# Performance work log

Hardware: AMD Instinct MI355X
Metric: run time of the kernel (lower is better)

Reference implementation:

```python
import jax, jax.numpy as jnp
import numpy as np

N_LAYERS = 2
D = 128


def _prelu(z, a):
    return jnp.where(z >= 0, z, a * z)


def _seg_sum(vals, idx, num):
    return jax.ops.segment_sum(vals, idx, num_segments=num)


def _conv_layer(x, ni, ei, Wn2e, bn2e, We2n, be2n, alpha, Dn_inv, De_inv, num_nodes, num_edges):
    # node -> edge: mean over member nodes (row norm), then linear + bias + PReLU
    e = _seg_sum((x @ Wn2e)[ni] * De_inv[ei][:, None], ei, num_edges) + bn2e
    e = _prelu(e, alpha)
    # edge -> node: mean over incident hyperedges
    n = _seg_sum((e @ We2n)[ei] * Dn_inv[ni][:, None], ni, num_nodes) + be2n
    return n, e


def _encoder(x, ni, ei, Wn2e, bn2e, We2n, be2n, alpha, Dn_inv, De_inv, num_nodes, num_edges):
    e = None
    for i in range(N_LAYERS):
        x, e = _conv_layer(x, ni, ei, Wn2e[i], bn2e[i], We2n[i], be2n[i], alpha, Dn_inv, De_inv, num_nodes, num_edges)
        x = _prelu(x, alpha)
    return x, e


def _decoder(x, e, ni, ei, We, Wx, b, alpha, Dn_inv, num_nodes):
    for i in range(N_LAYERS):
        m = _seg_sum((e @ We[i])[ei] * Dn_inv[ni][:, None], ni, num_nodes)
        x = _prelu(x @ Wx[i] + m + b[i], alpha)
    return x


def _forward(x, xx,
             e1_Wn2e, e1_bn2e, e1_We2n, e1_be2n,
             e2_Wn2e, e2_bn2e, e2_We2n, e2_be2n,
             d1_We, d1_Wx, d1_b, d2_We, d2_Wx, d2_b,
             alpha, node_idx, edge_idx, num_nodes, num_edges):
    # self loops: each node gets its own private hyperedge (id num_edges + node_id)
    ni = jnp.concatenate([node_idx, jnp.arange(num_nodes, dtype=node_idx.dtype)])
    ei = jnp.concatenate([edge_idx, jnp.arange(num_edges, num_edges + num_nodes, dtype=edge_idx.dtype)])
    ne_tot = num_edges + num_nodes
    ones = jnp.ones(ni.shape[0], x.dtype)
    Dn = _seg_sum(ones, ni, num_nodes)
    De = _seg_sum(ones, ei, ne_tot)
    Dn_inv = jnp.where(Dn > 0, 1.0 / Dn, 0.0)
    De_inv = jnp.where(De > 0, 1.0 / De, 0.0)

    n1, e1 = _encoder(x, ni, ei, e1_Wn2e, e1_bn2e, e1_We2n, e1_be2n, alpha, Dn_inv, De_inv, num_nodes, ne_tot)
    n2, e2 = _encoder(xx, ni, ei, e2_Wn2e, e2_bn2e, e2_We2n, e2_be2n, alpha, Dn_inv, De_inv, num_nodes, ne_tot)

    x11 = _decoder(n1, e1, ni, ei, d1_We, d1_Wx, d1_b, alpha, Dn_inv, num_nodes)
    x21 = _decoder(n2, e2, ni, ei, d2_We, d2_Wx, d2_b, alpha, Dn_inv, num_nodes)
    x12 = _decoder(n2, e2, ni, ei, d1_We, d1_Wx, d1_b, alpha, Dn_inv, num_nodes)
    x22 = _decoder(n1, e1, ni, ei, d2_We, d2_Wx, d2_b, alpha, Dn_inv, num_nodes)

    nn1 = jnp.concatenate([n1, n2], axis=1)
    return (nn1, n1, e1[:num_edges], n2, e2[:num_edges], x11, x21, x12, x22)


def setup_inputs() -> dict:
    key = jax.random.key(0)
    ks = jax.random.split(key, 24)
    N, E, NNZ = 50000, 20000, 800000
    s = 1.0 / np.sqrt(D)
    inp = {
        'x': jax.random.normal(ks[0], (N, D), jnp.float32),
        'xx': jax.random.normal(ks[1], (N, D), jnp.float32),
        'node_idx': jax.random.randint(ks[2], (NNZ,), 0, N, jnp.int32),
        'edge_idx': jax.random.randint(ks[3], (NNZ,), 0, E, jnp.int32),
        'num_nodes': N,
        'num_edges': E,
        'alpha': jnp.float32(0.25),
    }
    i = 4
    for enc in ('e1', 'e2'):
        inp[enc + '_Wn2e'] = jax.random.normal(ks[i], (N_LAYERS, D, D), jnp.float32) * s; i += 1
        inp[enc + '_bn2e'] = jnp.zeros((N_LAYERS, D), jnp.float32)
        inp[enc + '_We2n'] = jax.random.normal(ks[i], (N_LAYERS, D, D), jnp.float32) * s; i += 1
        inp[enc + '_be2n'] = jnp.zeros((N_LAYERS, D), jnp.float32)
    for dec in ('d1', 'd2'):
        inp[dec + '_We'] = jax.random.normal(ks[i], (N_LAYERS, D, D), jnp.float32) * s; i += 1
        inp[dec + '_Wx'] = jax.random.normal(ks[i], (N_LAYERS, D, D), jnp.float32) * s; i += 1
        inp[dec + '_b'] = jnp.zeros((N_LAYERS, D), jnp.float32)
    return inp


def reference(x, xx,
              e1_Wn2e, e1_bn2e, e1_We2n, e1_be2n,
              e2_Wn2e, e2_bn2e, e2_We2n, e2_be2n,
              d1_We, d1_Wx, d1_b, d2_We, d2_Wx, d2_b,
              alpha, node_idx, edge_idx, num_nodes, num_edges):
    return _forward(x, xx,
                    e1_Wn2e, e1_bn2e, e1_We2n, e1_be2n,
                    e2_Wn2e, e2_bn2e, e2_We2n, e2_be2n,
                    d1_We, d1_Wx, d1_b, d2_We, d2_Wx, d2_b,
                    alpha, node_idx, edge_idx, num_nodes, num_edges)
```

## Files before the change

kernel.cpp:

```cpp
#include <hip/hip_runtime.h>

#define DD 128

typedef __attribute__((ext_vector_type(8))) short bh8;
typedef __attribute__((ext_vector_type(8))) unsigned short us8;
typedef __attribute__((ext_vector_type(4))) float f4;
typedef unsigned int u32;
typedef unsigned short u16;

__device__ __forceinline__ u16 tob(float f) {
  u32 u = __builtin_bit_cast(u32, f);
  u += 0x7FFFu + ((u >> 16) & 1u);
  return (u16)(u >> 16);
}
__device__ __forceinline__ float fb(u16 h) { return __builtin_bit_cast(float, (u32)h << 16); }


__global__ __launch_bounds__(256) void init_counts_k(int* cn, int* ce, int N, int E) {
  int g = blockIdx.x * blockDim.x + threadIdx.x;
  if (g < E) ce[g] = 0;
  if (g < N) cn[g] = 0;
}


__global__ __launch_bounds__(256) void scan_partials_k(const int* __restrict__ cn, const int* __restrict__ ce,
                                                       int* part, int NCHN, int N, int NCHE, int E) {
  __shared__ int red[256];
  int b = blockIdx.x, tid = threadIdx.x;
  const int* cnt = (b < NCHN) ? cn : ce;
  int n = (b < NCHN) ? N : E;
  int base = ((b < NCHN) ? b : (b - NCHN)) << 10;
  int i0 = base + tid * 4;
  int s = 0;
  #pragma unroll
  for (int j = 0; j < 4; ++j) { int i = i0 + j; if (i < n) s += cnt[i]; }
  red[tid] = s; __syncthreads();
  for (int off = 128; off > 0; off >>= 1) {
    if (tid < off) red[tid] += red[tid + off];
    __syncthreads();
  }
  if (tid == 0) part[b] = red[0];
}

__device__ __forceinline__ int blk_excl_scan(int s, int tid, int* sums) {
  sums[tid] = s; __syncthreads();
  for (int off = 1; off < 256; off <<= 1) {
    int t = (tid >= off) ? sums[tid - off] : 0;
    __syncthreads();
    sums[tid] += t;
    __syncthreads();
  }
  int ex = sums[tid] - s;
  __syncthreads();
  return ex;
}

__global__ __launch_bounds__(256) void scan_apply_k(const int* __restrict__ cn, const int* __restrict__ ce,
                                                    const int* __restrict__ part,
                                                    int* offs_n, int* offs_e,
                                                    int NCHN, int N, int NCHE, int E) {
  __shared__ int sums[256];
  __shared__ int base_s;
  int b = blockIdx.x, tid = threadIdx.x;
  const bool isN = b < NCHN;
  const int* cnt = isN ? cn : ce;
  int* offs = isN ? offs_n : offs_e;
  int n = isN ? N : E;
  int nch = isN ? NCHN : NCHE;
  int c = isN ? b : b - NCHN;
  const int* pbase = isN ? part : part + NCHN;
  {
    int v = (tid < nch) ? pbase[tid] : 0;
    int ex = blk_excl_scan(v, tid, sums);
    if (tid == c) base_s = ex;
  }
  __syncthreads();
  int base = (c << 10);
  int i0 = base + tid * 4;
  int v[4]; int s = 0;
  #pragma unroll
  for (int j = 0; j < 4; ++j) { int i = i0 + j; int t = (i < n) ? cnt[i] : 0; v[j] = t; s += t; }
  int ex = blk_excl_scan(s, tid, sums);
  int run = base_s + ex;
  #pragma unroll
  for (int j = 0; j < 4; ++j) { int i = i0 + j; if (i < n) offs[i] = run; run += v[j]; }
  if (tid == 255 && base + 1024 >= n) offs[n] = run;
}

__global__ __launch_bounds__(256) void fill_deg_k(const int* __restrict__ offs_n, const int* __restrict__ offs_e,
                                                  float* Dn_inv, float* De_inv,
                                                  int* cur_be, int* cur_bn,
                                                  int N, int E, int NBE, int NBN) {
  int g = blockIdx.x * blockDim.x + threadIdx.x;
  if (g < E) {
    int b = offs_e[g], e = offs_e[g + 1];
    De_inv[g] = (e > b) ? 1.0f / (float)(e - b) : 0.0f;
  }
  if (g < N) {
    int b = offs_n[g], e = offs_n[g + 1];
    Dn_inv[g] = 1.0f / (float)(e - b + 1);
  }
  if (g < NBE) {
    int r1 = (g + 1) * 32; if (r1 > E) r1 = E;
    int o0 = offs_e[g * 32], o1 = offs_e[r1];
    int C = o1 - o0, base = 8 * o0;
    #pragma unroll
    for (int k = 0; k < 8; ++k) cur_be[g * 8 + k] = base + k * C;
  }
  if (g < NBN) {
    int r1 = (g + 1) * 32; if (r1 > N) r1 = N;
    int o0 = offs_n[g * 32], o1 = offs_n[r1];
    int C = o1 - o0, base = 8 * o0;
    #pragma unroll
    for (int k = 0; k < 8; ++k) cur_bn[g * 8 + k] = base + k * C;
  }
}

__global__ __launch_bounds__(256) void partition2_k(const int* __restrict__ ni, const int* __restrict__ ei,
                                                    int* cur_be, int* cur_bn,
                                                    u32* __restrict__ SE, u32* __restrict__ SN, int nnz) {
  int xcd;
  asm volatile("s_getreg_b32 %0, hwreg(HW_REG_XCC_ID)" : "=s"(xcd));
  xcd &= 7;
  int stride = gridDim.x * blockDim.x;
  for (int j = blockIdx.x * blockDim.x + threadIdx.x; j < nnz; j += stride) {
    int n = ni[j], e = ei[j];
    int pe = atomicAdd(&cur_be[(e >> 5) * 8 + xcd], 1);
    SE[pe] = ((u32)(e & 31) << 17) | (u32)n;
    int pn = atomicAdd(&cur_bn[(n >> 5) * 8 + xcd], 1);
    SN[pn] = ((u32)(n & 31) << 17) | (u32)e;
  }
}

__device__ __forceinline__ void scatter_body(const u32* __restrict__ S, const int* __restrict__ offs,
                                             const int* __restrict__ cur_b,
                                             int* __restrict__ list, int nRows, int b, int tid, int* cur) {
  const int i0 = b << 5;
  if (tid < 32) {
    int row = i0 + tid;
    cur[tid] = (row < nRows) ? offs[row] : 0;
  }
  __syncthreads();
  int r1 = i0 + 32; if (r1 > nRows) r1 = nRows;
  const int o0 = offs[i0];
  const int C = offs[r1] - o0;
  #pragma unroll 1
  for (int k = 0; k < 8; ++k) {
    int sbeg = 8 * o0 + k * C;
    int send = cur_b[b * 8 + k];
    for (int i = sbeg + tid; i < send; i += 256) {
      u32 v = S[i];
      int pos = atomicAdd(&cur[v >> 17], 1);
      list[pos] = (int)(v & 0x1FFFFu);
    }
  }
}

__global__ __launch_bounds__(256) void scatter_both_k(const u32* SE, const int* offs_e, const int* cur_be,
                                                      int* listE, int E, int NBE,
                                                      const u32* SN, const int* offs_n, const int* cur_bn,
                                                      int* listN, int N) {
  __shared__ int cur[32];
  int b = blockIdx.x, tid = threadIdx.x;
  if (b < NBE) scatter_body(SE, offs_e, cur_be, listE, E, b, tid, cur);
  else         scatter_body(SN, offs_n, cur_bn, listN, N, b - NBE, tid, cur);
}


__device__ __forceinline__ void acc8(float a[8], us8 v) {
  #pragma unroll
  for (int j = 0; j < 8; ++j) a[j] += fb(v[j]);
}

template<int SPLIT>
__global__ __launch_bounds__(256) void gather_edge_k(const u16* __restrict__ srcb,
                                                     const int* __restrict__ offs, const int* __restrict__ list,
                                                     const float* __restrict__ De_inv,
                                                     const float* __restrict__ b1, const float* __restrict__ b2,
                                                     const float* __restrict__ alphap,
                                                     u16* __restrict__ e_fullb,
                                                     float* __restrict__ d2a, float* __restrict__ d2b, int E) {
  const int wave = threadIdx.x >> 6, lane = threadIdx.x & 63;
  const int row = blockIdx.x * 4 + wave;
  if (row >= E) return;
  const int half = lane >> 5, cl = lane & 31;
  const int c8 = cl * 8;
  const int beg = offs[row], end = offs[row + 1];
  float a0[8] = {0,0,0,0,0,0,0,0}, a1[8] = {0,0,0,0,0,0,0,0};
  int i = beg + half;
  for (; i + 2 < end; i += 4) {
    us8 v0 = *(const us8*)&srcb[(size_t)list[i] * 256 + c8];
    us8 v1 = *(const us8*)&srcb[(size_t)list[i + 2] * 256 + c8];
    acc8(a0, v0); acc8(a1, v1);
  }
  if (i < end) acc8(a0, *(const us8*)&srcb[(size_t)list[i] * 256 + c8]);
  float s[8];
  #pragma unroll
  for (int j = 0; j < 8; ++j) s[j] = a0[j] + a1[j];
  #pragma unroll
  for (int j = 0; j < 8; ++j) s[j] += __shfl_xor(s[j], 32);
  if (half == 0) {
    float sc = De_inv[row];
    const float* bp = (c8 < 128) ? (b1 + c8) : (b2 + c8 - 128);
    float4 bt0 = *(const float4*)bp;
    float4 bt1 = *(const float4*)(bp + 4);
    float bb[8] = {bt0.x, bt0.y, bt0.z, bt0.w, bt1.x, bt1.y, bt1.z, bt1.w};
    float al = *alphap;
    us8 ob;
    float ov[8];
    #pragma unroll
    for (int j = 0; j < 8; ++j) {
      float v = sc * s[j] + bb[j];
      v = (v >= 0.f) ? v : al * v;
      ov[j] = v; ob[j] = tob(v);
    }
    *(us8*)&e_fullb[(size_t)row * 256 + c8] = ob;
    if constexpr (SPLIT == 1) {
      float* dp = (c8 < 128) ? &d2a[(size_t)row * DD + c8] : &d2b[(size_t)row * DD + c8 - 128];
      float4 w0 = {ov[0], ov[1], ov[2], ov[3]};
      float4 w1 = {ov[4], ov[5], ov[6], ov[7]};
      *(float4*)dp = w0;
      *(float4*)(dp + 4) = w1;
    }
  }
}

__global__ __launch_bounds__(256) void gather_node_k(const u16* __restrict__ e_fullb,
                                                     const u16* __restrict__ tb,
                                                     const int* __restrict__ offs, const int* __restrict__ list,
                                                     const float* __restrict__ Dn_inv,
                                                     const float* __restrict__ b1, const float* __restrict__ b2,
                                                     const float* __restrict__ alphap,
                                                     u16* __restrict__ dstb, int N) {
  const int wave = threadIdx.x >> 6, lane = threadIdx.x & 63;
  const int row = blockIdx.x * 4 + wave;
  if (row >= N) return;
  const int half = lane >> 5, cl = lane & 31;
  const int c8 = cl * 8;
  const int beg = offs[row], end = offs[row + 1];
  float a0[8] = {0,0,0,0,0,0,0,0}, a1[8] = {0,0,0,0,0,0,0,0};
  int i = beg + half;
  for (; i + 2 < end; i += 4) {
    us8 v0 = *(const us8*)&e_fullb[(size_t)list[i] * 256 + c8];
    us8 v1 = *(const us8*)&e_fullb[(size_t)list[i + 2] * 256 + c8];
    acc8(a0, v0); acc8(a1, v1);
  }
  if (i < end) acc8(a0, *(const us8*)&e_fullb[(size_t)list[i] * 256 + c8]);
  float s[8];
  #pragma unroll
  for (int j = 0; j < 8; ++j) s[j] = a0[j] + a1[j];
  #pragma unroll
  for (int j = 0; j < 8; ++j) s[j] += __shfl_xor(s[j], 32);
  if (half == 0) {
    us8 tv = *(const us8*)&tb[(size_t)row * 256 + c8];
    const float* bp = (c8 < 128) ? (b1 + c8) : (b2 + c8 - 128);
    float4 bt0 = *(const float4*)bp;
    float4 bt1 = *(const float4*)(bp + 4);
    float bb[8] = {bt0.x, bt0.y, bt0.z, bt0.w, bt1.x, bt1.y, bt1.z, bt1.w};
    float al = *alphap;
    float sc = Dn_inv[row];
    us8 ob;
    #pragma unroll
    for (int j = 0; j < 8; ++j) {
      float sv = fb(tv[j]) + bb[j];
      sv = (sv >= 0.f) ? sv : al * sv;
      ob[j] = tob(sc * (sv + s[j]));
    }
    *(us8*)&dstb[(size_t)row * 256 + c8] = ob;
  }
}


struct WPtrs { const float* p[16]; };

__global__ __launch_bounds__(256) void prep_w_k(WPtrs wp, char* dst) {
  int m = blockIdx.x >> 3, s = blockIdx.x & 7;
  const float* W = wp.p[m];
  int t = threadIdx.x;
  int n = t & 127;
  int k0 = s * 16 + (t >> 7) * 8;
  us8 vhi, vlo;
  #pragma unroll
  for (int j = 0; j < 8; ++j) {
    float x = W[(size_t)(k0 + j) * DD + n];
    u32 ux = __builtin_bit_cast(u32, x);
    float hf = __builtin_bit_cast(float, ux & 0xFFFF0000u);
    float l = x - hf;
    vhi[j] = (u16)(ux >> 16);
    vlo[j] = (u16)(__builtin_bit_cast(u32, l) >> 16);
  }
  char* base = dst + (size_t)m * 65536;
  int byte = n * 256 + k0 * 2;
  byte ^= (n & 7) << 4;
  *(us8*)(base + byte) = vhi;
  *(us8*)(base + 32768 + byte) = vlo;
}


__device__ __forceinline__ void stage_w(const char* gsrc, char* lds, int tid) {
  int wave = tid >> 6, lane = tid & 63;
  #pragma unroll
  for (int i = 0; i < 16; ++i) {
    int off = (wave * 16 + i) * 1024;
    __builtin_amdgcn_global_load_lds(
        (const __attribute__((address_space(1))) u32*)(gsrc + off + lane * 16),
        (__attribute__((address_space(3))) u32*)(lds + off), 16, 0, 0);
  }
}

__device__ __forceinline__ void stage_w32(const char* gsrc, char* lds, int tid) {
  int wave = tid >> 6, lane = tid & 63;
  #pragma unroll
  for (int i = 0; i < 8; ++i) {
    int off = (wave * 8 + i) * 1024;
    __builtin_amdgcn_global_load_lds(
        (const __attribute__((address_space(1))) u32*)(gsrc + off + lane * 16),
        (__attribute__((address_space(3))) u32*)(lds + off), 16, 0, 0);
  }
}

__device__ __forceinline__ void split8(const float vs[8], bh8& hi, bh8& lo) {
  #pragma unroll
  for (int j = 0; j < 8; ++j) {
    u32 u = __builtin_bit_cast(u32, vs[j]);
    float hf = __builtin_bit_cast(float, u & 0xFFFF0000u);
    float l = vs[j] - hf;
    hi[j] = (short)(u >> 16);
    lo[j] = (short)(__builtin_bit_cast(u32, l) >> 16);
  }
}

__device__ __forceinline__ void mk_afrag(const float* rowp, int koff, bh8& hi, bh8& lo) {
  float4 v0 = *(const float4*)(rowp + koff);
  float4 v1 = *(const float4*)(rowp + koff + 4);
  float vs[8] = {v0.x, v0.y, v0.z, v0.w, v1.x, v1.y, v1.z, v1.w};
  split8(vs, hi, lo);
}

__device__ __forceinline__ void mfma_ks(const bh8& ahi, const bh8& alo, const char* Wl,
                                        int ks, int lane, f4 acc[8]) {
  const int koff0 = (lane >> 4) * 8;
  const int k2 = (ks * 32 + koff0) * 2;
  #pragma unroll
  for (int cb = 0; cb < 8; ++cb) {
    int n = cb * 16 + (lane & 15);
    int byte = (n * 256 + k2) ^ ((n & 7) << 4);
    bh8 bhiF = *(const bh8*)(Wl + byte);
    bh8 bloF = *(const bh8*)(Wl + 32768 + byte);
    acc[cb] = __builtin_amdgcn_mfma_f32_16x16x32_bf16(ahi, bhiF, acc[cb], 0, 0, 0);
    acc[cb] = __builtin_amdgcn_mfma_f32_16x16x32_bf16(ahi, bloF, acc[cb], 0, 0, 0);
    acc[cb] = __builtin_amdgcn_mfma_f32_16x16x32_bf16(alo, bhiF, acc[cb], 0, 0, 0);
  }
}

__device__ __forceinline__ void mfma_ks_hi2(const bh8& ahi, const bh8& alo, const char* Wl,
                                            int ks, int lane, f4 acc[8]) {
  const int koff0 = (lane >> 4) * 8;
  const int k2 = (ks * 32 + koff0) * 2;
  #pragma unroll
  for (int cb = 0; cb < 8; ++cb) {
    int n = cb * 16 + (lane & 15);
    int byte = (n * 256 + k2) ^ ((n & 7) << 4);
    bh8 bhiF = *(const bh8*)(Wl + byte);
    acc[cb] = __builtin_amdgcn_mfma_f32_16x16x32_bf16(ahi, bhiF, acc[cb], 0, 0, 0);
    acc[cb] = __builtin_amdgcn_mfma_f32_16x16x32_bf16(alo, bhiF, acc[cb], 0, 0, 0);
  }
}

__device__ __forceinline__ void mfma_ks_bf(const bh8& a, const char* Wl,
                                           int ks, int lane, f4 acc[8]) {
  const int koff0 = (lane >> 4) * 8;
  const int k2 = (ks * 32 + koff0) * 2;
  #pragma unroll
  for (int cb = 0; cb < 8; ++cb) {
    int n = cb * 16 + (lane & 15);
    int byte = (n * 256 + k2) ^ ((n & 7) << 4);
    bh8 bhiF = *(const bh8*)(Wl + byte);
    bh8 bloF = *(const bh8*)(Wl + 32768 + byte);
    acc[cb] = __builtin_amdgcn_mfma_f32_16x16x32_bf16(a, bhiF, acc[cb], 0, 0, 0);
    acc[cb] = __builtin_amdgcn_mfma_f32_16x16x32_bf16(a, bloF, acc[cb], 0, 0, 0);
  }
}

__device__ __forceinline__ void mfma_ks_bfhi(const bh8& a, const char* Wl,
                                             int ks, int lane, f4 acc[8]) {
  const int koff0 = (lane >> 4) * 8;
  const int k2 = (ks * 32 + koff0) * 2;
  #pragma unroll
  for (int cb = 0; cb < 8; ++cb) {
    int n = cb * 16 + (lane & 15);
    int byte = (n * 256 + k2) ^ ((n & 7) << 4);
    bh8 bhiF = *(const bh8*)(Wl + byte);
    acc[cb] = __builtin_amdgcn_mfma_f32_16x16x32_bf16(a, bhiF, acc[cb], 0, 0, 0);
  }
}

__device__ __forceinline__ void mfma_passS_hi2(const float* __restrict__ A, size_t astride, int acoff,
                                               const char* Wl, int rbase, int nrows, int lane, f4 acc[8]) {
  int r = rbase + (lane & 15);
  if (r >= nrows) r = nrows - 1;
  const float* rowp = A + (size_t)r * astride + acoff;
  const int koff0 = (lane >> 4) * 8;
  #pragma unroll
  for (int ks = 0; ks < 4; ++ks) {
    bh8 ahi, alo;
    mk_afrag(rowp, ks * 32 + koff0, ahi, alo);
    mfma_ks_hi2(ahi, alo, Wl, ks, lane, acc);
  }
}

__device__ __forceinline__ void mfma_passB(const u16* __restrict__ A, size_t astride, int acoff,
                                           const char* Wl, int rbase, int nrows, int lane, f4 acc[8]) {
  int r = rbase + (lane & 15);
  if (r >= nrows) r = nrows - 1;
  const u16* rowp = A + (size_t)r * astride + acoff;
  const int koff0 = (lane >> 4) * 8;
  #pragma unroll
  for (int ks = 0; ks < 4; ++ks) {
    bh8 a = __builtin_bit_cast(bh8, *(const us8*)(rowp + ks * 32 + koff0));
    mfma_ks_bf(a, Wl, ks, lane, acc);
  }
}

__device__ __forceinline__ void mfma_passB_hi(const u16* __restrict__ A, size_t astride, int acoff,
                                              const char* Wl, int rbase, int nrows, int lane, f4 acc[8]) {
  int r = rbase + (lane & 15);
  if (r >= nrows) r = nrows - 1;
  const u16* rowp = A + (size_t)r * astride + acoff;
  const int koff0 = (lane >> 4) * 8;
  #pragma unroll
  for (int ks = 0; ks < 4; ++ks) {
    bh8 a = __builtin_bit_cast(bh8, *(const us8*)(rowp + ks * 32 + koff0));
    mfma_ks_bfhi(a, Wl, ks, lane, acc);
  }
}

struct AFragB { bh8 a[4]; };

__device__ __forceinline__ void load_afragB(const u16* __restrict__ A, size_t astride, int acoff,
                                            int rbase, int nrows, int lane, AFragB& f) {
  int r = rbase + (lane & 15);
  if (r >= nrows) r = nrows - 1;
  const u16* rowp = A + (size_t)r * astride + acoff;
  const int koff0 = (lane >> 4) * 8;
  #pragma unroll
  for (int ks = 0; ks < 4; ++ks)
    f.a[ks] = __builtin_bit_cast(bh8, *(const us8*)(rowp + ks * 32 + koff0));
}

__device__ __forceinline__ void mfma_pass_fragB(const AFragB& f, const char* Wl, int lane, f4 acc[8]) {
  #pragma unroll
  for (int ks = 0; ks < 4; ++ks) mfma_ks_bf(f.a[ks], Wl, ks, lane, acc);
}

__device__ __forceinline__ void mfma_pass_fragB_hi(const AFragB& f, const char* Wl, int lane, f4 acc[8]) {
  #pragma unroll
  for (int ks = 0; ks < 4; ++ks) mfma_ks_bfhi(f.a[ks], Wl, ks, lane, acc);
}


__device__ __forceinline__ void acc_to_T(f4 acc[8], const float* bias, float al,
                                         char* Tb, int wave, int lane) {
  const int cidx = lane & 15;
  float b8[8];
  #pragma unroll
  for (int cb = 0; cb < 8; ++cb) b8[cb] = bias[cb * 16 + cidx];
  #pragma unroll
  for (int q = 0; q < 4; ++q) {
    int row = wave * 16 + (lane >> 4) * 4 + q;
    #pragma unroll
    for (int cb = 0; cb < 8; ++cb) {
      float v = acc[cb][q] + b8[cb];
      v = (v >= 0.f) ? v : al * v;
      int byte = (row * 256 + (cb * 16 + cidx) * 2) ^ ((row & 7) << 4);
      *(u16*)(Tb + byte) = tob(v);
    }
  }
}

__device__ __forceinline__ void load_fT(const char* Tb, int wave, int lane, AFragB& f) {
  const int row = wave * 16 + (lane & 15);
  const int koff0 = (lane >> 4) * 8;
  #pragma unroll
  for (int ks = 0; ks < 4; ++ks) {
    int byte = (row * 256 + (ks * 32 + koff0) * 2) ^ ((row & 7) << 4);
    f.a[ks] = __builtin_bit_cast(bh8, *(const us8*)(Tb + byte));
  }
}

template<int MODE, int OBF>
__device__ __forceinline__ void epilogueS(f4 acc[8], const float* bias, const float* alphap,
                                          void* outp, size_t ostride, int ocoff,
                                          int rbase, int nrows, int lane) {
  float al = 0.f;
  if constexpr (MODE == 1) al = *alphap;
  const int cidx = lane & 15;
  int rq = rbase + (lane >> 4) * 4;
  float b8[8];
  if constexpr (MODE == 1) {
    #pragma unroll
    for (int cb = 0; cb < 8; ++cb) b8[cb] = bias[cb * 16 + cidx];
  }
  #pragma unroll
  for (int q = 0; q < 4; ++q) {
    int row = rq + q;
    if (row < nrows) {
      #pragma unroll
      for (int cb = 0; cb < 8; ++cb) {
        float v = acc[cb][q];
        if constexpr (MODE == 1) { v += b8[cb]; v = (v >= 0.f) ? v : al * v; }
        if constexpr (OBF == 1) {
          u16* op = (u16*)outp + (size_t)row * ostride + ocoff + cidx;
          op[cb * 16] = tob(v);
        } else {
          float* op = (float*)outp + (size_t)row * ostride + ocoff + cidx;
          op[cb * 16] = v;
        }
      }
    }
  }
}

#define ACC_ZERO(acc) { _Pragma("unroll") for (int cb = 0; cb < 8; ++cb) acc[cb] = {0.f, 0.f, 0.f, 0.f}; }


__global__ __launch_bounds__(256, 2) void combo1_k(const float* __restrict__ x, const char* W0,
                                                   const float* __restrict__ xx, const char* W4,
                                                   u16* __restrict__ tb, int nrows, int NT,
                                                   const int* __restrict__ ni, const int* __restrict__ ei,
                                                   int* cn, int* ce, int nnz) {
  __shared__ char Wl[32768];
  if ((int)blockIdx.x < NT) {
    const int wave = threadIdx.x >> 6, lane = threadIdx.x & 63;
    const int rbase = blockIdx.x * 64 + wave * 16;
    f4 acc[8];
    stage_w32(W0, Wl, threadIdx.x);
    __syncthreads();
    ACC_ZERO(acc);
    mfma_passS_hi2(x, DD, 0, Wl, rbase, nrows, lane, acc);
    epilogueS<0, 1>(acc, nullptr, nullptr, tb, 256, 0, rbase, nrows, lane);
    __syncthreads();
    stage_w32(W4, Wl, threadIdx.x);
    __syncthreads();
    ACC_ZERO(acc);
    mfma_passS_hi2(xx, DD, 0, Wl, rbase, nrows, lane, acc);
    epilogueS<0, 1>(acc, nullptr, nullptr, tb, 256, 128, rbase, nrows, lane);
  } else {
    int nb = gridDim.x - NT;
    int stride = nb * 256;
    for (int j = ((int)blockIdx.x - NT) * 256 + (int)threadIdx.x; j < nnz; j += stride) {
      atomicAdd(&cn[ni[j]], 1);
      atomicAdd(&ce[ei[j]], 1);
    }
  }
}

__global__ __launch_bounds__(256, 2) void gemm_fuse_hid_k(const u16* __restrict__ thb,
                                                          const char* W20, const float* b20, const char* W21,
                                                          const char* W60, const float* b60, const char* W61,
                                                          const float* __restrict__ alphap,
                                                          u16* __restrict__ tb_out, int nrows) {
  __shared__ char Wl[81920];
  char* H0 = Wl;
  char* H1 = Wl + 32768;
  char* Tb = Wl + 65536;
  const int wave = threadIdx.x >> 6, lane = threadIdx.x & 63;
  const int rbase = blockIdx.x * 64 + wave * 16;
  const float al = *alphap;
  f4 acc[8];
  AFragB fT;
  #pragma unroll 1
  for (int h = 0; h < 2; ++h) {
    if (h) __syncthreads();
    stage_w32(h ? W60 : W20, H0, threadIdx.x);
    __syncthreads();
    stage_w32(h ? W61 : W21, H1, threadIdx.x);
    ACC_ZERO(acc);
    mfma_passB_hi(thb, 256, h * 128, H0, rbase, nrows, lane, acc);
    __syncthreads();
    acc_to_T(acc, h ? b60 : b20, al, Tb, wave, lane);
    __syncthreads();
    load_fT(Tb, wave, lane, fT);
    ACC_ZERO(acc);
    mfma_pass_fragB_hi(fT, H1, lane, acc);
    epilogueS<0, 1>(acc, nullptr, nullptr, tb_out, 256, h * 128, rbase, nrows, lane);
  }
}

__global__ __launch_bounds__(256, 2) void enc_final_k(const u16* __restrict__ aggb, const char* W1, const float* b1_,
                                                      const char* W2, const float* b2_,
                                                      const float* __restrict__ alphap,
                                                      float* __restrict__ n1, float* __restrict__ n2,
                                                      u16* __restrict__ n1b, u16* __restrict__ n2b,
                                                      float* __restrict__ nn1, int nrows) {
  __shared__ char Wl[65536];
  const int wave = threadIdx.x >> 6, lane = threadIdx.x & 63;
  const int rbase = blockIdx.x * 64 + wave * 16;
  const int cidx = lane & 15;
  f4 acc[8];
  float al = *alphap;
  #pragma unroll 1
  for (int h = 0; h < 2; ++h) {
    if (h) __syncthreads();
    stage_w(h ? W2 : W1, Wl, threadIdx.x);
    __syncthreads();
    const float* bp = h ? b2_ : b1_;
    float* nout = h ? n2 : n1;
    u16* nbout = h ? n2b : n1b;
    float b8[8];
    #pragma unroll
    for (int cb = 0; cb < 8; ++cb) b8[cb] = bp[cb * 16 + cidx];
    ACC_ZERO(acc);
    mfma_passB(aggb, 256, h * 128, Wl, rbase, nrows, lane, acc);
    int rq = rbase + (lane >> 4) * 4;
    #pragma unroll
    for (int q = 0; q < 4; ++q) {
      int row = rq + q;
      if (row < nrows) {
        float* op = nout + (size_t)row * DD + cidx;
        float* op2 = nn1 + (size_t)row * 256 + h * 128 + cidx;
        u16* op3 = nbout + (size_t)row * DD + cidx;
        #pragma unroll
        for (int cb = 0; cb < 8; ++cb) {
          float v = acc[cb][q] + b8[cb];
          v = (v >= 0.f) ? v : al * v;
          op[cb * 16] = v;
          op2[cb * 16] = v;
          op3[cb * 16] = tob(v);
        }
      }
    }
  }
}

__global__ __launch_bounds__(256, 2) void dec_fused_k(const u16* __restrict__ n1b, const u16* __restrict__ n2b,
                                                      const u16* __restrict__ aggb,
                                                      const char* Wx10, const char* We10, const float* b1_0,
                                                      const char* Wx11, const char* We11, const float* b1_1,
                                                      const char* Wx20, const char* We20, const float* b2_0,
                                                      const char* Wx21, const char* We21, const float* b2_1,
                                                      const float* __restrict__ alphap,
                                                      float* __restrict__ x11, float* __restrict__ x22,
                                                      float* __restrict__ x12, float* __restrict__ x21,
                                                      int nrows) {
  __shared__ char Wl[65536];
  const int y = blockIdx.y;
  const u16* xb = y ? n2b : n1b;
  float* od1 = y ? x12 : x11;
  float* od2 = y ? x21 : x22;
  const int acoff = y * 128;
  const int wave = threadIdx.x >> 6, lane = threadIdx.x & 63;
  const int rbase = blockIdx.x * 64 + wave * 16;
  const float al = *alphap;
  AFragB fx, fa, fT;
  load_afragB(xb, DD, 0, rbase, nrows, lane, fx);
  load_afragB(aggb, 256, acoff, rbase, nrows, lane, fa);
  f4 acc[8];
  #pragma unroll 1
  for (int s = 0; s < 2; ++s) {
    const char* Wx0 = s ? Wx20 : Wx10;
    const char* We0 = s ? We20 : We10;
    const char* Wx1 = s ? Wx21 : Wx11;
    const char* We1 = s ? We21 : We11;
    const float* b0 = s ? b2_0 : b1_0;
    const float* b1 = s ? b2_1 : b1_1;
    float* out = s ? od2 : od1;
    if (s) __syncthreads();
    stage_w(Wx0, Wl, threadIdx.x);
    __syncthreads();
    ACC_ZERO(acc);
    mfma_pass_fragB(fx, Wl, lane, acc);
    __syncthreads();
    stage_w(We0, Wl, threadIdx.x);
    __syncthreads();
    mfma_pass_fragB(fa, Wl, lane, acc);
    __syncthreads();
    acc_to_T(acc, b0, al, Wl, wave, lane);
    __syncthreads();
    load_fT(Wl, wave, lane, fT);
    __syncthreads();
    stage_w(Wx1, Wl, threadIdx.x);
    __syncthreads();
    ACC_ZERO(acc);
    mfma_pass_fragB(fT, Wl, lane, acc);
    __syncthreads();
    stage_w(We1, Wl, threadIdx.x);
    __syncthreads();
    mfma_pass_fragB(fa, Wl, lane, acc);
    epilogueS<1, 0>(acc, b1, alphap, out, DD, 0, rbase, nrows, lane);
  }
}


extern "C" void kernel_launch(void* const* d_in, const int* in_sizes, int n_in,
                              void* d_out, int out_size, void* d_ws, size_t ws_size,
                              hipStream_t stream) {
  const float* x        = (const float*)d_in[0];
  const float* xx       = (const float*)d_in[1];
  const int*   node_idx = (const int*)d_in[2];
  const int*   edge_idx = (const int*)d_in[3];
  const float* alphap   = (const float*)d_in[6];
  const float* e1_Wn2e  = (const float*)d_in[7];
  const float* e1_bn2e  = (const float*)d_in[8];
  const float* e1_We2n  = (const float*)d_in[9];
  const float* e1_be2n  = (const float*)d_in[10];
  const float* e2_Wn2e  = (const float*)d_in[11];
  const float* e2_bn2e  = (const float*)d_in[12];
  const float* e2_We2n  = (const float*)d_in[13];
  const float* e2_be2n  = (const float*)d_in[14];
  const float* d1_We    = (const float*)d_in[15];
  const float* d1_Wx    = (const float*)d_in[16];
  const float* d1_b     = (const float*)d_in[17];
  const float* d2_We    = (const float*)d_in[18];
  const float* d2_Wx    = (const float*)d_in[19];
  const float* d2_b     = (const float*)d_in[20];

  const int N   = in_sizes[0] / DD;
  const int NNZ = in_sizes[2];
  const int E   = (out_size - 1024 * N) / 256;
  const int NBE = (E + 31) >> 5;
  const int NBN = (N + 31) >> 5;
  const int NCHN = (N + 1023) >> 10;
  const int NCHE = (E + 1023) >> 10;

  float* out  = (float*)d_out;
  float* nn1  = out;
  float* n1   = out + (size_t)N * 256;
  float* e1o  = n1 + (size_t)N * DD;
  float* n2   = e1o + (size_t)E * DD;
  float* e2o  = n2 + (size_t)N * DD;
  float* x11  = e2o + (size_t)E * DD;
  float* x21  = x11 + (size_t)N * DD;
  float* x12  = x21 + (size_t)N * DD;
  float* x22  = x12 + (size_t)N * DD;

  size_t off = 0;
  char* w0 = (char*)d_ws;
  auto carve = [&](size_t bytes) -> void* {
    void* p = (void*)(w0 + off);
    off += (bytes + 255) & ~(size_t)255;
    return p;
  };
  int* cn      = (int*)carve((size_t)N * 4);
  int* ce      = (int*)carve((size_t)E * 4);
  int* offs_n  = (int*)carve((size_t)(N + 1) * 4);
  int* offs_e  = (int*)carve((size_t)(E + 1) * 4);
  int* part    = (int*)carve((size_t)(NCHN + NCHE) * 4);
  int* listN   = (int*)carve((size_t)NNZ * 4);
  int* listE   = (int*)carve((size_t)NNZ * 4);
  float* Dn_inv = (float*)carve((size_t)N * 4);
  float* De_inv = (float*)carve((size_t)E * 4);
  char* Wprep  = (char*)carve((size_t)16 * 65536);
  u16* tb      = (u16*)carve((size_t)N * 256 * 2);
  u16* e_fullb = (u16*)carve((size_t)E * 256 * 2);
  u16* thb     = (u16*)carve((size_t)N * 256 * 2);
  u16* aggb    = (u16*)carve((size_t)N * 256 * 2);
  u16* n1b     = (u16*)carve((size_t)N * DD * 2);
  u16* n2b     = (u16*)carve((size_t)N * DD * 2);
  int* cur_be  = (int*)carve((size_t)NBE * 8 * 4);
  int* cur_bn  = (int*)carve((size_t)NBN * 8 * 4);
  u32* SE      = (u32*)carve((size_t)NNZ * 8 * 4);
  u32* SN      = (u32*)carve((size_t)NNZ * 8 * 4);

  WPtrs wp;
  wp.p[0] = e1_Wn2e;  wp.p[1] = e1_Wn2e + DD * DD;
  wp.p[2] = e1_We2n;  wp.p[3] = e1_We2n + DD * DD;
  wp.p[4] = e2_Wn2e;  wp.p[5] = e2_Wn2e + DD * DD;
  wp.p[6] = e2_We2n;  wp.p[7] = e2_We2n + DD * DD;
  wp.p[8] = d1_We;    wp.p[9] = d1_We + DD * DD;
  wp.p[10] = d1_Wx;   wp.p[11] = d1_Wx + DD * DD;
  wp.p[12] = d2_We;   wp.p[13] = d2_We + DD * DD;
  wp.p[14] = d2_Wx;   wp.p[15] = d2_Wx + DD * DD;
  auto WP = [&](int i) -> const char* { return Wprep + (size_t)i * 65536; };

  const int thr = 256;
  const int gMax = ((N > E ? N : E) + thr - 1) / thr;
  const int NT = (N + 63) / 64;
  const int HB = 512;
  int gNNZ = (NNZ + thr - 1) / thr; if (gNNZ > 2048) gNNZ = 2048;
  const int gGatE = (E + 3) / 4;
  const int gGatN = (N + 3) / 4;

  prep_w_k<<<128, 256, 0, stream>>>(wp, Wprep);
  init_counts_k<<<gMax, thr, 0, stream>>>(cn, ce, N, E);
  combo1_k<<<NT + HB, 256, 0, stream>>>(x, WP(0), xx, WP(4), tb, N, NT,
                                        node_idx, edge_idx, cn, ce, NNZ);
  scan_partials_k<<<NCHN + NCHE, 256, 0, stream>>>(cn, ce, part, NCHN, N, NCHE, E);
  scan_apply_k<<<NCHN + NCHE, 256, 0, stream>>>(cn, ce, part, offs_n, offs_e, NCHN, N, NCHE, E);
  fill_deg_k<<<gMax, thr, 0, stream>>>(offs_n, offs_e, Dn_inv, De_inv,
                                       cur_be, cur_bn, N, E, NBE, NBN);
  partition2_k<<<gNNZ, thr, 0, stream>>>(node_idx, edge_idx, cur_be, cur_bn, SE, SN, NNZ);
  scatter_both_k<<<NBE + NBN, 256, 0, stream>>>(SE, offs_e, cur_be, listE, E, NBE,
                                                SN, offs_n, cur_bn, listN, N);

  gather_edge_k<0><<<gGatE, 256, 0, stream>>>(tb, offs_e, listE, De_inv, e1_bn2e, e2_bn2e,
                                              alphap, e_fullb, nullptr, nullptr, E);
  gather_node_k<<<gGatN, 256, 0, stream>>>(e_fullb, tb, offs_n, listN, Dn_inv, e1_bn2e, e2_bn2e,
                                           alphap, thb, N);
  gemm_fuse_hid_k<<<NT, 256, 0, stream>>>(thb, WP(2), e1_be2n, WP(1),
                                          WP(6), e2_be2n, WP(5), alphap, tb, N);
  gather_edge_k<1><<<gGatE, 256, 0, stream>>>(tb, offs_e, listE, De_inv, e1_bn2e + DD, e2_bn2e + DD,
                                              alphap, e_fullb, e1o, e2o, E);
  gather_node_k<<<gGatN, 256, 0, stream>>>(e_fullb, tb, offs_n, listN, Dn_inv, e1_bn2e + DD, e2_bn2e + DD,
                                           alphap, aggb, N);
  enc_final_k<<<NT, 256, 0, stream>>>(aggb, WP(3), e1_be2n + DD, WP(7), e2_be2n + DD,
                                      alphap, n1, n2, n1b, n2b, nn1, N);

  dim3 gDec(NT, 2);
  dec_fused_k<<<gDec, 256, 0, stream>>>(n1b, n2b, aggb,
                                        WP(10), WP(8), d1_b, WP(11), WP(9), d1_b + DD,
                                        WP(14), WP(12), d2_b, WP(15), WP(13), d2_b + DD,
                                        alphap, x11, x22, x12, x21, N);
}
```

Baseline: 566.4 us.

## Fold degree fill into scan and split first GEMM across count and partition kernels

Drops the fill_deg kernel: scan_apply now writes Dn_inv/De_inv straight from the counts and computes the per-bucket cursor bases from its shared scan sums. The first encoder GEMM is split in half. One half runs alongside the count atomics and the other alongside the partition scatter, so that GEMM work overlaps the atomic-bound phases. This saves one launch and balances the work across two kernels, but the cursor derivation depends on the 32-row bucket lining up with eight threads of four rows each.

```diff
diff --git a/kernel.cpp b/kernel.cpp
--- a/kernel.cpp
+++ b/kernel.cpp
@@ -21,7 +21,6 @@
   if (g < E) ce[g] = 0;
   if (g < N) cn[g] = 0;
 }
-
 
 __global__ __launch_bounds__(256) void scan_partials_k(const int* __restrict__ cn, const int* __restrict__ ce,
                                                        int* part, int NCHN, int N, int NCHE, int E) {
@@ -58,7 +57,9 @@
 __global__ __launch_bounds__(256) void scan_apply_k(const int* __restrict__ cn, const int* __restrict__ ce,
                                                     const int* __restrict__ part,
                                                     int* offs_n, int* offs_e,
-                                                    int NCHN, int N, int NCHE, int E) {
+                                                    float* Dn_inv, float* De_inv,
+                                                    int* cur_bn, int* cur_be,
+                                                    int NCHN, int N, int NCHE, int E, int NBN, int NBE) {
   __shared__ int sums[256];
   __shared__ int base_s;
   int b = blockIdx.x, tid = threadIdx.x;
@@ -83,52 +84,29 @@
   int ex = blk_excl_scan(s, tid, sums);
   int run = base_s + ex;
   #pragma unroll
-  for (int j = 0; j < 4; ++j) { int i = i0 + j; if (i < n) offs[i] = run; run += v[j]; }
+  for (int j = 0; j < 4; ++j) {
+    int i = i0 + j;
+    if (i < n) {
+      offs[i] = run;
+      if (isN) Dn_inv[i] = 1.0f / (float)(v[j] + 1);
+      else     De_inv[i] = (v[j] > 0) ? 1.0f / (float)v[j] : 0.0f;
+      run += v[j];
+    }
+  }
   if (tid == 255 && base + 1024 >= n) offs[n] = run;
-}
-
-__global__ __launch_bounds__(256) void fill_deg_k(const int* __restrict__ offs_n, const int* __restrict__ offs_e,
-                                                  float* Dn_inv, float* De_inv,
-                                                  int* cur_be, int* cur_bn,
-                                                  int N, int E, int NBE, int NBN) {
-  int g = blockIdx.x * blockDim.x + threadIdx.x;
-  if (g < E) {
-    int b = offs_e[g], e = offs_e[g + 1];
-    De_inv[g] = (e > b) ? 1.0f / (float)(e - b) : 0.0f;
-  }
-  if (g < N) {
-    int b = offs_n[g], e = offs_n[g + 1];
-    Dn_inv[g] = 1.0f / (float)(e - b + 1);
-  }
-  if (g < NBE) {
-    int r1 = (g + 1) * 32; if (r1 > E) r1 = E;
-    int o0 = offs_e[g * 32], o1 = offs_e[r1];
-    int C = o1 - o0, base = 8 * o0;
-    #pragma unroll
-    for (int k = 0; k < 8; ++k) cur_be[g * 8 + k] = base + k * C;
-  }
-  if (g < NBN) {
-    int r1 = (g + 1) * 32; if (r1 > N) r1 = N;
-    int o0 = offs_n[g * 32], o1 = offs_n[r1];
-    int C = o1 - o0, base = 8 * o0;
-    #pragma unroll
-    for (int k = 0; k < 8; ++k) cur_bn[g * 8 + k] = base + k * C;
-  }
-}
-
-__global__ __launch_bounds__(256) void partition2_k(const int* __restrict__ ni, const int* __restrict__ ei,
-                                                    int* cur_be, int* cur_bn,
-                                                    u32* __restrict__ SE, u32* __restrict__ SN, int nnz) {
-  int xcd;
-  asm volatile("s_getreg_b32 %0, hwreg(HW_REG_XCC_ID)" : "=s"(xcd));
-  xcd &= 7;
-  int stride = gridDim.x * blockDim.x;
-  for (int j = blockIdx.x * blockDim.x + threadIdx.x; j < nnz; j += stride) {
-    int n = ni[j], e = ei[j];
-    int pe = atomicAdd(&cur_be[(e >> 5) * 8 + xcd], 1);
-    SE[pe] = ((u32)(e & 31) << 17) | (u32)n;
-    int pn = atomicAdd(&cur_bn[(n >> 5) * 8 + xcd], 1);
-    SN[pn] = ((u32)(n & 31) << 17) | (u32)e;
+  if (tid < 32) {
+    int gb = c * 32 + tid;
+    int NB = isN ? NBN : NBE;
+    if (gb < NB) {
+      int t0 = tid * 8;
+      int pre = t0 ? sums[t0 - 1] : 0;
+      int o0 = base_s + pre;
+      int C = sums[t0 + 7] - pre;
+      int* cur = isN ? cur_bn : cur_be;
+      int b8 = 8 * o0;
+      #pragma unroll
+      for (int k = 0; k < 8; ++k) cur[gb * 8 + k] = b8 + k * C;
+    }
   }
 }
 
@@ -337,22 +315,6 @@
   split8(vs, hi, lo);
 }
 
-__device__ __forceinline__ void mfma_ks(const bh8& ahi, const bh8& alo, const char* Wl,
-                                        int ks, int lane, f4 acc[8]) {
-  const int koff0 = (lane >> 4) * 8;
-  const int k2 = (ks * 32 + koff0) * 2;
-  #pragma unroll
-  for (int cb = 0; cb < 8; ++cb) {
-    int n = cb * 16 + (lane & 15);
-    int byte = (n * 256 + k2) ^ ((n & 7) << 4);
-    bh8 bhiF = *(const bh8*)(Wl + byte);
-    bh8 bloF = *(const bh8*)(Wl + 32768 + byte);
-    acc[cb] = __builtin_amdgcn_mfma_f32_16x16x32_bf16(ahi, bhiF, acc[cb], 0, 0, 0);
-    acc[cb] = __builtin_amdgcn_mfma_f32_16x16x32_bf16(ahi, bloF, acc[cb], 0, 0, 0);
-    acc[cb] = __builtin_amdgcn_mfma_f32_16x16x32_bf16(alo, bhiF, acc[cb], 0, 0, 0);
-  }
-}
-
 __device__ __forceinline__ void mfma_ks_hi2(const bh8& ahi, const bh8& alo, const char* Wl,
                                             int ks, int lane, f4 acc[8]) {
   const int koff0 = (lane >> 4) * 8;
@@ -524,33 +486,64 @@
 #define ACC_ZERO(acc) { _Pragma("unroll") for (int cb = 0; cb < 8; ++cb) acc[cb] = {0.f, 0.f, 0.f, 0.f}; }
 
 
-__global__ __launch_bounds__(256, 2) void combo1_k(const float* __restrict__ x, const char* W0,
-                                                   const float* __restrict__ xx, const char* W4,
-                                                   u16* __restrict__ tb, int nrows, int NT,
-                                                   const int* __restrict__ ni, const int* __restrict__ ei,
-                                                   int* cn, int* ce, int nnz) {
+__device__ __forceinline__ void gemm1_body(const float* __restrict__ x, const char* W0,
+                                           const float* __restrict__ xx, const char* W4,
+                                           u16* __restrict__ tb, int nrows, int blk, char* Wl) {
+  const int wave = threadIdx.x >> 6, lane = threadIdx.x & 63;
+  const int rbase = blk * 64 + wave * 16;
+  f4 acc[8];
+  stage_w32(W0, Wl, threadIdx.x);
+  __syncthreads();
+  ACC_ZERO(acc);
+  mfma_passS_hi2(x, DD, 0, Wl, rbase, nrows, lane, acc);
+  epilogueS<0, 1>(acc, nullptr, nullptr, tb, 256, 0, rbase, nrows, lane);
+  __syncthreads();
+  stage_w32(W4, Wl, threadIdx.x);
+  __syncthreads();
+  ACC_ZERO(acc);
+  mfma_passS_hi2(xx, DD, 0, Wl, rbase, nrows, lane, acc);
+  epilogueS<0, 1>(acc, nullptr, nullptr, tb, 256, 128, rbase, nrows, lane);
+}
+
+__global__ __launch_bounds__(256, 2) void combo_a_k(const float* __restrict__ x, const char* W0,
+                                                    const float* __restrict__ xx, const char* W4,
+                                                    u16* __restrict__ tb, int nrows, int NTg,
+                                                    const int* __restrict__ ni, const int* __restrict__ ei,
+                                                    int* cn, int* ce, int nnz) {
   __shared__ char Wl[32768];
-  if ((int)blockIdx.x < NT) {
-    const int wave = threadIdx.x >> 6, lane = threadIdx.x & 63;
-    const int rbase = blockIdx.x * 64 + wave * 16;
-    f4 acc[8];
-    stage_w32(W0, Wl, threadIdx.x);
-    __syncthreads();
-    ACC_ZERO(acc);
-    mfma_passS_hi2(x, DD, 0, Wl, rbase, nrows, lane, acc);
-    epilogueS<0, 1>(acc, nullptr, nullptr, tb, 256, 0, rbase, nrows, lane);
-    __syncthreads();
-    stage_w32(W4, Wl, threadIdx.x);
-    __syncthreads();
-    ACC_ZERO(acc);
-    mfma_passS_hi2(xx, DD, 0, Wl, rbase, nrows, lane, acc);
-    epilogueS<0, 1>(acc, nullptr, nullptr, tb, 256, 128, rbase, nrows, lane);
+  if ((int)blockIdx.x < NTg) {
+    gemm1_body(x, W0, xx, W4, tb, nrows, blockIdx.x, Wl);
   } else {
-    int nb = gridDim.x - NT;
+    int nb = gridDim.x - NTg;
     int stride = nb * 256;
-    for (int j = ((int)blockIdx.x - NT) * 256 + (int)threadIdx.x; j < nnz; j += stride) {
+    for (int j = ((int)blockIdx.x - NTg) * 256 + (int)threadIdx.x; j < nnz; j += stride) {
       atomicAdd(&cn[ni[j]], 1);
       atomicAdd(&ce[ei[j]], 1);
+    }
+  }
+}
+
+__global__ __launch_bounds__(256, 2) void combo_b_k(const float* __restrict__ x, const char* W0,
+                                                    const float* __restrict__ xx, const char* W4,
+                                                    u16* __restrict__ tb, int nrows, int NTg, int blk0,
+                                                    const int* __restrict__ ni, const int* __restrict__ ei,
+                                                    int* cur_be, int* cur_bn,
+                                                    u32* __restrict__ SE, u32* __restrict__ SN, int nnz) {
+  __shared__ char Wl[32768];
+  if ((int)blockIdx.x < NTg) {
+    gemm1_body(x, W0, xx, W4, tb, nrows, blk0 + blockIdx.x, Wl);
+  } else {
+    int xcd;
+    asm volatile("s_getreg_b32 %0, hwreg(HW_REG_XCC_ID)" : "=s"(xcd));
+    xcd &= 7;
+    int nb = gridDim.x - NTg;
+    int stride = nb * 256;
+    for (int j = ((int)blockIdx.x - NTg) * 256 + (int)threadIdx.x; j < nnz; j += stride) {
+      int n = ni[j], e = ei[j];
+      int pe = atomicAdd(&cur_be[(e >> 5) * 8 + xcd], 1);
+      SE[pe] = ((u32)(e & 31) << 17) | (u32)n;
+      int pn = atomicAdd(&cur_bn[(n >> 5) * 8 + xcd], 1);
+      SN[pn] = ((u32)(n & 31) << 17) | (u32)e;
     }
   }
 }
@@ -776,20 +769,23 @@
   const int thr = 256;
   const int gMax = ((N > E ? N : E) + thr - 1) / thr;
   const int NT = (N + 63) / 64;
+  const int NTa = NT / 2;
+  const int NTb = NT - NTa;
   const int HB = 512;
-  int gNNZ = (NNZ + thr - 1) / thr; if (gNNZ > 2048) gNNZ = 2048;
+  const int PB = 512;
   const int gGatE = (E + 3) / 4;
   const int gGatN = (N + 3) / 4;
 
   prep_w_k<<<128, 256, 0, stream>>>(wp, Wprep);
   init_counts_k<<<gMax, thr, 0, stream>>>(cn, ce, N, E);
-  combo1_k<<<NT + HB, 256, 0, stream>>>(x, WP(0), xx, WP(4), tb, N, NT,
-                                        node_idx, edge_idx, cn, ce, NNZ);
+  combo_a_k<<<NTa + HB, 256, 0, stream>>>(x, WP(0), xx, WP(4), tb, N, NTa,
+                                          node_idx, edge_idx, cn, ce, NNZ);
   scan_partials_k<<<NCHN + NCHE, 256, 0, stream>>>(cn, ce, part, NCHN, N, NCHE, E);
-  scan_apply_k<<<NCHN + NCHE, 256, 0, stream>>>(cn, ce, part, offs_n, offs_e, NCHN, N, NCHE, E);
-  fill_deg_k<<<gMax, thr, 0, stream>>>(offs_n, offs_e, Dn_inv, De_inv,
-                                       cur_be, cur_bn, N, E, NBE, NBN);
-  partition2_k<<<gNNZ, thr, 0, stream>>>(node_idx, edge_idx, cur_be, cur_bn, SE, SN, NNZ);
+  scan_apply_k<<<NCHN + NCHE, 256, 0, stream>>>(cn, ce, part, offs_n, offs_e,
+                                                Dn_inv, De_inv, cur_bn, cur_be,
+                                                NCHN, N, NCHE, E, NBN, NBE);
+  combo_b_k<<<NTb + PB, 256, 0, stream>>>(x, WP(0), xx, WP(4), tb, N, NTb, NTa,
+                                          node_idx, edge_idx, cur_be, cur_bn, SE, SN, NNZ);
   scatter_both_k<<<NBE + NBN, 256, 0, stream>>>(SE, offs_e, cur_be, listE, E, NBE,
                                                 SN, offs_n, cur_bn, listN, N);
 
```

Measured after the change: 558.4 us. About the same (-1.4%).
